# Kernel tuning notes

Measured on AMD Instinct MI355X. Metric: run time of the kernel, lower is better.

Reference implementation:

```python
import jax, jax.numpy as jnp
import numpy as np

EPS = 1e-6
SMOOTH = 0.025


def setup_inputs() -> dict:
    key = jax.random.key(0)
    k1, = jax.random.split(key, 1)
    x = jax.random.uniform(k1, (32, 128, 8000), dtype=jnp.float32)  # (B, C, T) energies >= 0
    alpha = jnp.float32(0.98)
    delta = jnp.float32(2.0)
    r = jnp.float32(0.5)
    return {"x": x, "alpha": alpha, "delta": delta, "r": r}


def reference(x, alpha, delta, r):
    # x: (B, C, T)
    x = jnp.maximum(x, 0.0)
    xt = jnp.moveaxis(x, -1, 0)  # (T, B, C) for time scan

    def ema_step(M, xt_t):
        M = (1.0 - SMOOTH) * M + SMOOTH * xt_t
        return M, M

    M0 = jnp.zeros(x.shape[:2], dtype=x.dtype)  # (B, C)
    _, Mt = jax.lax.scan(ema_step, M0, xt)  # (T, B, C)
    M = jnp.moveaxis(Mt, 0, -1)  # (B, C, T)

    norm = x / jnp.power(EPS + M, alpha)
    y = jnp.power(norm + delta, r) - jnp.power(delta, r)
    return y
```

## Files before the change

kernel.cpp:

```cpp
#include <hip/hip_runtime.h>

#define EPSV   1e-6f
#define SMOOTH 0.025f
#define HALF   4096
#define WARM   512

typedef float v4f __attribute__((ext_vector_type(4)));

__device__ __forceinline__ float fast_log2(float v) { return __builtin_amdgcn_logf(v); }
__device__ __forceinline__ float fast_exp2(float v) { return __builtin_amdgcn_exp2f(v); }

__device__ __forceinline__ float pcen_elem(float xr, float M, float nalpha,
                                           float delta, float r, float dr) {
    float m    = EPSV + M;
    float norm = xr * fast_exp2(nalpha * fast_log2(m));
    return fast_exp2(r * fast_log2(norm + delta)) - dr;
}

struct KC {
    float a1, a2, a3, a4;
    float e0, e1, e2, e3, e4, e5;
    float a4lane;
    float a256;
    int   lane;
};

__device__ __forceinline__ void scan_group(const KC& c,
                                           const float xa[4], const float xb[4],
                                           float& m0, float Ma[4], float Mb[4]) {
    const float b = SMOOTH;
    float qa0 = b * xa[0];
    float qa1 = fmaf(c.a1, qa0, b * xa[1]);
    float qa2 = fmaf(c.a1, qa1, b * xa[2]);
    float qa3 = fmaf(c.a1, qa2, b * xa[3]);
    float qb0 = b * xb[0];
    float qb1 = fmaf(c.a1, qb0, b * xb[1]);
    float qb2 = fmaf(c.a1, qb1, b * xb[2]);
    float qb3 = fmaf(c.a1, qb2, b * xb[3]);

    float PA = qa3, PB = qb3, u;
    u = __shfl_up(PA, 1, 64);  PA = fmaf(c.lane >= 1  ? c.e0 : 0.f, u, PA);
    u = __shfl_up(PB, 1, 64);  PB = fmaf(c.lane >= 1  ? c.e0 : 0.f, u, PB);
    u = __shfl_up(PA, 2, 64);  PA = fmaf(c.lane >= 2  ? c.e1 : 0.f, u, PA);
    u = __shfl_up(PB, 2, 64);  PB = fmaf(c.lane >= 2  ? c.e1 : 0.f, u, PB);
    u = __shfl_up(PA, 4, 64);  PA = fmaf(c.lane >= 4  ? c.e2 : 0.f, u, PA);
    u = __shfl_up(PB, 4, 64);  PB = fmaf(c.lane >= 4  ? c.e2 : 0.f, u, PB);
    u = __shfl_up(PA, 8, 64);  PA = fmaf(c.lane >= 8  ? c.e3 : 0.f, u, PA);
    u = __shfl_up(PB, 8, 64);  PB = fmaf(c.lane >= 8  ? c.e3 : 0.f, u, PB);
    u = __shfl_up(PA, 16, 64); PA = fmaf(c.lane >= 16 ? c.e4 : 0.f, u, PA);
    u = __shfl_up(PB, 16, 64); PB = fmaf(c.lane >= 16 ? c.e4 : 0.f, u, PB);
    u = __shfl_up(PA, 32, 64); PA = fmaf(c.lane >= 32 ? c.e5 : 0.f, u, PA);
    u = __shfl_up(PB, 32, 64); PB = fmaf(c.lane >= 32 ? c.e5 : 0.f, u, PB);

    float TA = __shfl(PA, 63, 64);
    float TB = __shfl(PB, 63, 64);
    float PexcA = __shfl_up(PA, 1, 64); if (c.lane == 0) PexcA = 0.f;
    float PexcB = __shfl_up(PB, 1, 64); if (c.lane == 0) PexcB = 0.f;

    float mA = m0;
    float mB = fmaf(c.a256, m0, TA);
    m0       = fmaf(c.a256, mB, TB);

    float sA = fmaf(c.a4lane, mA, PexcA);
    float sB = fmaf(c.a4lane, mB, PexcB);
    Ma[0] = fmaf(c.a1, sA, qa0);
    Ma[1] = fmaf(c.a2, sA, qa1);
    Ma[2] = fmaf(c.a3, sA, qa2);
    Ma[3] = fmaf(c.a4, sA, qa3);
    Mb[0] = fmaf(c.a1, sB, qb0);
    Mb[1] = fmaf(c.a2, sB, qb1);
    Mb[2] = fmaf(c.a3, sB, qb2);
    Mb[3] = fmaf(c.a4, sB, qb3);
}

__global__ __launch_bounds__(256, 6) void pcen_ema_kernel(
    const float* __restrict__ x,
    const float* __restrict__ alpha_p,
    const float* __restrict__ delta_p,
    const float* __restrict__ r_p,
    float* __restrict__ y,
    int rows, int T)
{
    const int gid   = blockIdx.x * blockDim.x + threadIdx.x;
    const int wave  = gid >> 6;
    const int lane  = gid & 63;
    const int row   = wave >> 1;
    const int chunk = wave & 1;
    if (row >= rows) return;

    const float nalpha = -alpha_p[0];
    const float delta  = delta_p[0];
    const float r      = r_p[0];
    const float dr     = fast_exp2(r * fast_log2(delta));

    KC c;
    c.lane = lane;
    const float a = 1.0f - SMOOTH;
    c.a1 = a;  c.a2 = a * a;  c.a3 = c.a2 * a;  c.a4 = c.a2 * c.a2;
    c.e0 = c.a4;      c.e1 = c.e0 * c.e0;  c.e2 = c.e1 * c.e1;
    c.e3 = c.e2 * c.e2; c.e4 = c.e3 * c.e3; c.e5 = c.e4 * c.e4;
    c.a256 = c.e5 * c.e5;
    float a4l = 1.0f;
    if (lane & 1)  a4l *= c.e0;
    if (lane & 2)  a4l *= c.e1;
    if (lane & 4)  a4l *= c.e2;
    if (lane & 8)  a4l *= c.e3;
    if (lane & 16) a4l *= c.e4;
    if (lane & 32) a4l *= c.e5;
    c.a4lane = a4l;

    const long long base = (long long)row * T;
    const float* __restrict__ xrow = x + base;
    float* __restrict__       yrow = y + base;

    const int tstart = chunk ? HALF : 0;
    const int tend   = chunk ? T    : HALF;
    const int off    = 4 * lane;

    float m0 = 0.0f;

    if (chunk) {
        const int tw = HALF - WARM;
        v4f wa = *(const v4f*)(xrow + tw + off);
        v4f wb = *(const v4f*)(xrow + tw + 256 + off);
        float xa[4] = { fmaxf(wa.x,0.f), fmaxf(wa.y,0.f), fmaxf(wa.z,0.f), fmaxf(wa.w,0.f) };
        float xb[4] = { fmaxf(wb.x,0.f), fmaxf(wb.y,0.f), fmaxf(wb.z,0.f), fmaxf(wb.w,0.f) };
        float Ma[4], Mb[4];
        scan_group(c, xa, xb, m0, Ma, Mb);
    }

    const int nfull = (tend - tstart) >> 9;
    int t = tstart;

    v4f va = {0,0,0,0}, vb = va;
    if (nfull > 0) {
        va = *(const v4f*)(xrow + t + off);
        vb = *(const v4f*)(xrow + t + 256 + off);
    }
    for (int i = 0; i < nfull; ++i) {
        const int tn = t + 512;
        const int tp = (i + 1 < nfull) ? tn : t;
        v4f na = *(const v4f*)(xrow + tp + off);
        v4f nb = *(const v4f*)(xrow + tp + 256 + off);

        float xa[4] = { fmaxf(va.x,0.f), fmaxf(va.y,0.f), fmaxf(va.z,0.f), fmaxf(va.w,0.f) };
        float xb[4] = { fmaxf(vb.x,0.f), fmaxf(vb.y,0.f), fmaxf(vb.z,0.f), fmaxf(vb.w,0.f) };
        float Ma[4], Mb[4];
        scan_group(c, xa, xb, m0, Ma, Mb);

        v4f oa, ob;
        oa.x = pcen_elem(xa[0], Ma[0], nalpha, delta, r, dr);
        oa.y = pcen_elem(xa[1], Ma[1], nalpha, delta, r, dr);
        oa.z = pcen_elem(xa[2], Ma[2], nalpha, delta, r, dr);
        oa.w = pcen_elem(xa[3], Ma[3], nalpha, delta, r, dr);
        ob.x = pcen_elem(xb[0], Mb[0], nalpha, delta, r, dr);
        ob.y = pcen_elem(xb[1], Mb[1], nalpha, delta, r, dr);
        ob.z = pcen_elem(xb[2], Mb[2], nalpha, delta, r, dr);
        ob.w = pcen_elem(xb[3], Mb[3], nalpha, delta, r, dr);
        __builtin_nontemporal_store(oa, (v4f*)(yrow + t + off));
        __builtin_nontemporal_store(ob, (v4f*)(yrow + t + 256 + off));

        va = na; vb = nb; t = tn;
    }

    if (t < tend) {
        float xa[4], xb[4];
        #pragma unroll
        for (int k = 0; k < 4; ++k) {
            int ia = t + off + k;
            int ib = t + 256 + off + k;
            xa[k] = (ia < tend) ? fmaxf(xrow[ia], 0.f) : 0.f;
            xb[k] = (ib < tend) ? fmaxf(xrow[ib], 0.f) : 0.f;
        }
        float Ma[4], Mb[4];
        scan_group(c, xa, xb, m0, Ma, Mb);
        #pragma unroll
        for (int k = 0; k < 4; ++k) {
            int ia = t + off + k;
            int ib = t + 256 + off + k;
            if (ia < tend) yrow[ia] = pcen_elem(xa[k], Ma[k], nalpha, delta, r, dr);
            if (ib < tend) yrow[ib] = pcen_elem(xb[k], Mb[k], nalpha, delta, r, dr);
        }
    }
}

extern "C" void kernel_launch(void* const* d_in, const int* in_sizes, int n_in,
                              void* d_out, int out_size, void* d_ws, size_t ws_size,
                              hipStream_t stream) {
    const float* x     = (const float*)d_in[0];
    const float* alpha = (const float*)d_in[1];
    const float* delta = (const float*)d_in[2];
    const float* r     = (const float*)d_in[3];
    float* y = (float*)d_out;

    const int T     = 8000;
    const int total = in_sizes[0];
    const int rows  = total / T;

    const int waves   = rows * 2;
    const int threads = waves * 64;
    const int block   = 256;
    const int grid    = (threads + block - 1) / block;
    pcen_ema_kernel<<<grid, block, 0, stream>>>(x, alpha, delta, r, y, rows, T);
}
```

Baseline: 46.92 us.

## Add sqrt fast path for r=0.5, asm nontemporal stores, vectorized tail

```diff
diff --git a/kernel.cpp b/kernel.cpp
--- a/kernel.cpp
+++ b/kernel.cpp
@@ -10,11 +10,9 @@
 __device__ __forceinline__ float fast_log2(float v) { return __builtin_amdgcn_logf(v); }
 __device__ __forceinline__ float fast_exp2(float v) { return __builtin_amdgcn_exp2f(v); }
 
-__device__ __forceinline__ float pcen_elem(float xr, float M, float nalpha,
-                                           float delta, float r, float dr) {
-    float m    = EPSV + M;
-    float norm = xr * fast_exp2(nalpha * fast_log2(m));
-    return fast_exp2(r * fast_log2(norm + delta)) - dr;
+__device__ __forceinline__ void store_nt16(float* p, v4f v) {
+    asm volatile("global_store_dwordx4 %0, %1, off sc0 sc1 nt"
+                 :: "v"(p), "v"(v) : "memory");
 }
 
 struct KC {
@@ -73,7 +71,12 @@
     Mb[3] = fmaf(c.a4, sB, qb3);
 }
 
-__global__ __launch_bounds__(256, 6) void pcen_ema_kernel(
+__device__ __forceinline__ float pcen_norm(float xr, float M, float nalpha, float delta) {
+    float m = EPSV + M;
+    return fmaf(xr, fast_exp2(nalpha * fast_log2(m)), delta);
+}
+
+__global__ __launch_bounds__(256, 8) void pcen_ema_kernel(
     const float* __restrict__ x,
     const float* __restrict__ alpha_p,
     const float* __restrict__ delta_p,
@@ -91,14 +94,16 @@
     const float nalpha = -alpha_p[0];
     const float delta  = delta_p[0];
     const float r      = r_p[0];
-    const float dr     = fast_exp2(r * fast_log2(delta));
+    const bool  rhalf  = (r == 0.5f);
+    const float dr     = rhalf ? __builtin_sqrtf(delta)
+                               : fast_exp2(r * fast_log2(delta));
 
     KC c;
     c.lane = lane;
     const float a = 1.0f - SMOOTH;
     c.a1 = a;  c.a2 = a * a;  c.a3 = c.a2 * a;  c.a4 = c.a2 * c.a2;
-    c.e0 = c.a4;      c.e1 = c.e0 * c.e0;  c.e2 = c.e1 * c.e1;
-    c.e3 = c.e2 * c.e2; c.e4 = c.e3 * c.e3; c.e5 = c.e4 * c.e4;
+    c.e0 = c.a4;        c.e1 = c.e0 * c.e0;  c.e2 = c.e1 * c.e1;
+    c.e3 = c.e2 * c.e2; c.e4 = c.e3 * c.e3;  c.e5 = c.e4 * c.e4;
     c.a256 = c.e5 * c.e5;
     float a4l = 1.0f;
     if (lane & 1)  a4l *= c.e0;
@@ -148,39 +153,74 @@
         float Ma[4], Mb[4];
         scan_group(c, xa, xb, m0, Ma, Mb);
 
+        float pa[4], pb[4];
+        #pragma unroll
+        for (int k = 0; k < 4; ++k) pa[k] = pcen_norm(xa[k], Ma[k], nalpha, delta);
+        #pragma unroll
+        for (int k = 0; k < 4; ++k) pb[k] = pcen_norm(xb[k], Mb[k], nalpha, delta);
+
         v4f oa, ob;
-        oa.x = pcen_elem(xa[0], Ma[0], nalpha, delta, r, dr);
-        oa.y = pcen_elem(xa[1], Ma[1], nalpha, delta, r, dr);
-        oa.z = pcen_elem(xa[2], Ma[2], nalpha, delta, r, dr);
-        oa.w = pcen_elem(xa[3], Ma[3], nalpha, delta, r, dr);
-        ob.x = pcen_elem(xb[0], Mb[0], nalpha, delta, r, dr);
-        ob.y = pcen_elem(xb[1], Mb[1], nalpha, delta, r, dr);
-        ob.z = pcen_elem(xb[2], Mb[2], nalpha, delta, r, dr);
-        ob.w = pcen_elem(xb[3], Mb[3], nalpha, delta, r, dr);
-        __builtin_nontemporal_store(oa, (v4f*)(yrow + t + off));
-        __builtin_nontemporal_store(ob, (v4f*)(yrow + t + 256 + off));
+        if (rhalf) {
+            oa.x = __builtin_sqrtf(pa[0]) - dr;
+            oa.y = __builtin_sqrtf(pa[1]) - dr;
+            oa.z = __builtin_sqrtf(pa[2]) - dr;
+            oa.w = __builtin_sqrtf(pa[3]) - dr;
+            ob.x = __builtin_sqrtf(pb[0]) - dr;
+            ob.y = __builtin_sqrtf(pb[1]) - dr;
+            ob.z = __builtin_sqrtf(pb[2]) - dr;
+            ob.w = __builtin_sqrtf(pb[3]) - dr;
+        } else {
+            oa.x = fast_exp2(r * fast_log2(pa[0])) - dr;
+            oa.y = fast_exp2(r * fast_log2(pa[1])) - dr;
+            oa.z = fast_exp2(r * fast_log2(pa[2])) - dr;
+            oa.w = fast_exp2(r * fast_log2(pa[3])) - dr;
+            ob.x = fast_exp2(r * fast_log2(pb[0])) - dr;
+            ob.y = fast_exp2(r * fast_log2(pb[1])) - dr;
+            ob.z = fast_exp2(r * fast_log2(pb[2])) - dr;
+            ob.w = fast_exp2(r * fast_log2(pb[3])) - dr;
+        }
+        store_nt16(yrow + t + off, oa);
+        store_nt16(yrow + t + 256 + off, ob);
 
         va = na; vb = nb; t = tn;
     }
 
     if (t < tend) {
-        float xa[4], xb[4];
-        #pragma unroll
-        for (int k = 0; k < 4; ++k) {
-            int ia = t + off + k;
-            int ib = t + 256 + off + k;
-            xa[k] = (ia < tend) ? fmaxf(xrow[ia], 0.f) : 0.f;
-            xb[k] = (ib < tend) ? fmaxf(xrow[ib], 0.f) : 0.f;
-        }
+        const int offA = t + off;
+        const int offB = t + 256 + off;
+        const int la = offA < tend - 4 ? offA : tend - 4;
+        const int lb = offB < tend - 4 ? offB : tend - 4;
+        v4f wa = *(const v4f*)(xrow + la);
+        v4f wb = *(const v4f*)(xrow + lb);
+        float xa[4] = { fmaxf(wa.x,0.f), fmaxf(wa.y,0.f), fmaxf(wa.z,0.f), fmaxf(wa.w,0.f) };
+        float xb[4] = { fmaxf(wb.x,0.f), fmaxf(wb.y,0.f), fmaxf(wb.z,0.f), fmaxf(wb.w,0.f) };
         float Ma[4], Mb[4];
         scan_group(c, xa, xb, m0, Ma, Mb);
-        #pragma unroll
-        for (int k = 0; k < 4; ++k) {
-            int ia = t + off + k;
-            int ib = t + 256 + off + k;
-            if (ia < tend) yrow[ia] = pcen_elem(xa[k], Ma[k], nalpha, delta, r, dr);
-            if (ib < tend) yrow[ib] = pcen_elem(xb[k], Mb[k], nalpha, delta, r, dr);
+
+        float pa[4], pb[4];
+        #pragma unroll
+        for (int k = 0; k < 4; ++k) pa[k] = pcen_norm(xa[k], Ma[k], nalpha, delta);
+        #pragma unroll
+        for (int k = 0; k < 4; ++k) pb[k] = pcen_norm(xb[k], Mb[k], nalpha, delta);
+
+        v4f oa, ob;
+        if (rhalf) {
+            oa.x = __builtin_sqrtf(pa[0]) - dr;  oa.y = __builtin_sqrtf(pa[1]) - dr;
+            oa.z = __builtin_sqrtf(pa[2]) - dr;  oa.w = __builtin_sqrtf(pa[3]) - dr;
+            ob.x = __builtin_sqrtf(pb[0]) - dr;  ob.y = __builtin_sqrtf(pb[1]) - dr;
+            ob.z = __builtin_sqrtf(pb[2]) - dr;  ob.w = __builtin_sqrtf(pb[3]) - dr;
+        } else {
+            oa.x = fast_exp2(r * fast_log2(pa[0])) - dr;
+            oa.y = fast_exp2(r * fast_log2(pa[1])) - dr;
+            oa.z = fast_exp2(r * fast_log2(pa[2])) - dr;
+            oa.w = fast_exp2(r * fast_log2(pa[3])) - dr;
+            ob.x = fast_exp2(r * fast_log2(pb[0])) - dr;
+            ob.y = fast_exp2(r * fast_log2(pb[1])) - dr;
+            ob.z = fast_exp2(r * fast_log2(pb[2])) - dr;
+            ob.w = fast_exp2(r * fast_log2(pb[3])) - dr;
         }
+        if (offA + 4 <= tend) store_nt16(yrow + offA, oa);
+        if (offB + 4 <= tend) store_nt16(yrow + offB, ob);
     }
 }
 
```

After: 48.08 us. 2.5% more time.
